# Optimization experiments

Measured on AMD Instinct MI355X. Metric: run time of the kernel, lower is better.

The kernel has to match this reference:

```python
import jax, jax.numpy as jnp
import numpy as np

B, S, H = 2, 2048, 2048
NH, NKV, D = 32, 8, 64
N_REP = NH // NKV  # 4
THETA = 10000.0


def _rotate_half(x):
    x1, x2 = jnp.split(x, 2, axis=-1)
    return jnp.concatenate([-x2, x1], axis=-1)


def _apply_rope(q, k, position_ids):
    # q: [B,NH,S,D], k: [B,NKV,S,D], position_ids: [B,S]
    inv_freq = 1.0 / (THETA ** (jnp.arange(0, D, 2, dtype=jnp.float32) / D))  # [D/2]
    ang = position_ids[:, None, :, None].astype(jnp.float32) * inv_freq      # [B,1,S,D/2]
    cos = jnp.concatenate([jnp.cos(ang), jnp.cos(ang)], axis=-1)             # [B,1,S,D]
    sin = jnp.concatenate([jnp.sin(ang), jnp.sin(ang)], axis=-1)
    q = q * cos + _rotate_half(q) * sin
    k = k * cos + _rotate_half(k) * sin
    return q, k


def setup_inputs() -> dict:
    key = jax.random.key(0)
    k1, k2, k3, k4 = jax.random.split(key, 4)
    hidden_states = jax.random.normal(k1, (B, S, H), dtype=jnp.float32)
    position_ids = jnp.broadcast_to(jnp.arange(S, dtype=jnp.int64 if jax.config.jax_enable_x64 else jnp.int32)[None, :], (B, S))
    Wq = jax.random.normal(k2, (H, NH * D), dtype=jnp.float32) * 0.02
    Wkv = jax.random.normal(k3, (H, NKV * 2 * D), dtype=jnp.float32) * 0.02
    Wo = jax.random.normal(k4, (H, H), dtype=jnp.float32) * 0.02
    return {"hidden_states": hidden_states, "position_ids": position_ids,
            "Wq": Wq, "Wkv": Wkv, "Wo": Wo}


def reference(hidden_states, position_ids, Wq, Wkv, Wo):
    b, s, _ = hidden_states.shape
    # fused QKV projections (Linear, no bias)
    q = (hidden_states @ Wq).reshape(b, s, NH, D).transpose(0, 2, 1, 3)      # [B,NH,S,D]
    kv = (hidden_states @ Wkv).reshape(b, s, NKV, 2, D)
    k = kv[:, :, :, 0, :].transpose(0, 2, 1, 3)                              # [B,NKV,S,D]
    v = kv[:, :, :, 1, :].transpose(0, 2, 1, 3)                              # [B,NKV,S,D]
    # rotary embedding
    q, k = _apply_rope(q, k, position_ids)
    # GQA: repeat_interleave K/V heads
    k = jnp.repeat(k, N_REP, axis=1)                                         # [B,NH,S,D]
    v = jnp.repeat(v, N_REP, axis=1)
    # causal SDPA (eval mode: dropout_p = 0)
    scale = 1.0 / np.sqrt(D)
    scores = jnp.einsum('bhqd,bhkd->bhqk', q, k) * scale                     # [B,NH,S,S]
    causal = jnp.tril(jnp.ones((s, s), dtype=bool))
    scores = jnp.where(causal[None, None], scores, jnp.finfo(scores.dtype).min)
    probs = jax.nn.softmax(scores, axis=-1)
    ctx = jnp.einsum('bhqk,bhkd->bhqd', probs, v)                            # [B,NH,S,D]
    ctx = ctx.transpose(0, 2, 1, 3).reshape(b, s, H)
    return ctx @ Wo
```

## Files before the change

kernel.cpp:

```cpp
#include <hip/hip_runtime.h>

typedef __bf16 bf16_t;
typedef __bf16 bf16x8 __attribute__((ext_vector_type(8)));
typedef __bf16 bf16x4 __attribute__((ext_vector_type(4)));
typedef float f32x4 __attribute__((ext_vector_type(4)));

#define DEV static __device__ __forceinline__

DEV void gload16(const void* g, void* lds) {
  __builtin_amdgcn_global_load_lds((__attribute__((address_space(1))) void*)g,
                                   (__attribute__((address_space(3))) void*)lds, 16, 0, 0);
}

DEV f32x4 mfma16(bf16x8 a, bf16x8 b, f32x4 c) {
  return __builtin_amdgcn_mfma_f32_16x16x32_bf16(a, b, c, 0, 0, 0);
}

__global__ __launch_bounds__(256) void k_cvt_bf16(const float* __restrict__ in,
                                                  bf16_t* __restrict__ out, int n) {
  int i = (blockIdx.x * 256 + threadIdx.x) * 4;
  if (i + 3 < n) {
    float4 v = *(const float4*)(in + i);
    bf16x4 o;
    o[0] = (bf16_t)v.x; o[1] = (bf16_t)v.y; o[2] = (bf16_t)v.z; o[3] = (bf16_t)v.w;
    *(bf16x4*)(out + i) = o;
  }
}

__global__ __launch_bounds__(256) void k_transpose(const float* __restrict__ in,
                                                   bf16_t* __restrict__ out, int R, int C) {
  __shared__ float tile[32][33];
  const int tx = threadIdx.x & 31, ty = threadIdx.x >> 5;
  const int rb = blockIdx.y * 32, cb = blockIdx.x * 32;
#pragma unroll
  for (int i = 0; i < 32; i += 8)
    tile[ty + i][tx] = in[(size_t)(rb + ty + i) * C + (cb + tx)];
  __syncthreads();
#pragma unroll
  for (int i = 0; i < 32; i += 8)
    out[(size_t)(cb + ty + i) * R + (rb + tx)] = (bf16_t)tile[tx][ty + i];
}

__global__ __launch_bounds__(256) void k_rope_table(const int* __restrict__ pos_ids,
                                                    float2* __restrict__ tbl) {
  const int token = blockIdx.x * 8 + (threadIdx.x >> 5);
  const int d2 = threadIdx.x & 31;
  const float p = (float)pos_ids[token];
  const float freq = exp2f(-(float)d2 / 32.0f * log2f(10000.0f));
  const float a = p * freq;
  tbl[token * 32 + d2] = make_float2(cosf(a), sinf(a));
}

#define STAGE_A(bi, st, h)                                                      \
  do {                                                                          \
    const bf16_t* _s = gA + (size_t)(brow + (h) * 128 + r0) * gK + (st) * 64 + l0 * 8; \
    gload16(_s, &As[bi][((h) * 1024 + tid) * 8]);                               \
    gload16(_s + (size_t)64 * gK, &As[bi][((h) * 1024 + 512 + tid) * 8]);       \
  } while (0)

#define STAGE_B(bi, st, h)                                                      \
  do {                                                                          \
    const bf16_t* _s = gB + (size_t)(bcol + (h) * 128 + r0) * gK + (st) * 64 + l0 * 8; \
    gload16(_s, &Bs[bi][((h) * 1024 + tid) * 8]);                               \
    gload16(_s + (size_t)64 * gK, &Bs[bi][((h) * 1024 + 512 + tid) * 8]);       \
  } while (0)

#define LOADA(bi, mh)                                                           \
  _Pragma("unroll")                                                             \
  for (int mq = 0; mq < 4; ++mq) {                                              \
    const int R = wm * 128 + (mh) * 64 + mq * 16 + c15;                         \
    af[mq][0] = *(const bf16x8*)(&As[bi][(R * 8 + (g ^ (R & 7))) * 8]);         \
    af[mq][1] = *(const bf16x8*)(&As[bi][(R * 8 + ((4 + g) ^ (R & 7))) * 8]);   \
  }

#define LOADB(bi, nh)                                                           \
  _Pragma("unroll")                                                             \
  for (int nq = 0; nq < 2; ++nq) {                                              \
    const int R = wn * 64 + ((nh) * 2 + nq) * 16 + c15;                         \
    bfr[nq][0] = *(const bf16x8*)(&Bs[bi][(R * 8 + (g ^ (R & 7))) * 8]);        \
    bfr[nq][1] = *(const bf16x8*)(&Bs[bi][(R * 8 + ((4 + g) ^ (R & 7))) * 8]);  \
  }

#define MFMAQ(mh, nh)                                                           \
  _Pragma("unroll")                                                             \
  for (int nq = 0; nq < 2; ++nq)                                                \
    _Pragma("unroll")                                                           \
    for (int mq = 0; mq < 4; ++mq)                                              \
      acc[(mh) * 4 + mq][(nh) * 2 + nq] =                                       \
          mfma16(af[mq][1], bfr[nq][1],                                         \
                 mfma16(af[mq][0], bfr[nq][0], acc[(mh) * 4 + mq][(nh) * 2 + nq]));

#define PH_MID()                                            \
  __builtin_amdgcn_s_barrier();                             \
  asm volatile("s_waitcnt lgkmcnt(0)" ::: "memory");        \
  __builtin_amdgcn_sched_barrier(0);                        \
  __builtin_amdgcn_s_setprio(1)

#define PH_END()                                            \
  __builtin_amdgcn_s_setprio(0);                            \
  __builtin_amdgcn_s_barrier()

template <int MODE>
__global__ __launch_bounds__(512, 2) void k_gemm256(
    const bf16_t* __restrict__ gA, const bf16_t* __restrict__ gB,
    int gK, int NBX,
    float* __restrict__ C, int ldc,
    const float2* __restrict__ tbl,
    bf16_t* __restrict__ Qp, bf16_t* __restrict__ Kp, bf16_t* __restrict__ Vt) {
  __shared__ __align__(16) bf16_t As[2][256 * 64];
  __shared__ __align__(16) bf16_t Bs[2][256 * 64];
  const int tid = threadIdx.x;
  const int lane = tid & 63, w = tid >> 6;
  const int c15 = lane & 15, g = lane >> 4;
  const int wm = w >> 2, wn = w & 3;

  const int cpx = (int)gridDim.x >> 3;
  const int u = ((int)blockIdx.x & 7) * cpx + ((int)blockIdx.x >> 3);
  const int bx = u % NBX, by = u / NBX;
  const int brow = by * 256, bcol = bx * 256;

  const int r0 = tid >> 3, p0 = tid & 7;
  const int l0 = p0 ^ (r0 & 7);

  const f32x4 fzero = {0.f, 0.f, 0.f, 0.f};
  f32x4 acc[8][4];
#pragma unroll
  for (int m = 0; m < 8; ++m)
#pragma unroll
    for (int n = 0; n < 4; ++n) acc[m][n] = fzero;

  const int NT = gK >> 6;

  STAGE_A(0, 0, 0); STAGE_A(0, 0, 1); STAGE_B(0, 0, 0); STAGE_B(0, 0, 1);
  STAGE_A(1, 1, 0);
  asm volatile("s_waitcnt vmcnt(2)" ::: "memory");
  __builtin_amdgcn_s_barrier();

  for (int t = 0; t < NT; ++t) {
    const int bi = t & 1, oi = bi ^ 1;
    const int st1 = (t + 1 < NT) ? t + 1 : NT - 1;
    const int st2 = (t + 2 < NT) ? t + 2 : NT - 1;
    bf16x8 af[4][2], bfr[2][2];

    LOADA(bi, 0);
    LOADB(bi, 0);
    STAGE_A(oi, st1, 1);
    STAGE_B(oi, st1, 0);
    PH_MID();
    MFMAQ(0, 0);
    PH_END();

    LOADB(bi, 1);
    STAGE_B(oi, st1, 1);
    PH_MID();
    MFMAQ(0, 1);
    PH_END();

    LOADA(bi, 1);
    LOADB(bi, 0);
    PH_MID();
    MFMAQ(1, 0);
    PH_END();

    LOADB(bi, 1);
    STAGE_A(bi, st2, 0);
    asm volatile("s_waitcnt vmcnt(2)" ::: "memory");
    PH_MID();
    MFMAQ(1, 1);
    PH_END();
  }

  if constexpr (MODE == 0) {
#pragma unroll
    for (int m = 0; m < 8; ++m)
#pragma unroll
      for (int n = 0; n < 4; ++n)
#pragma unroll
        for (int r = 0; r < 4; ++r) {
          const int row = brow + wm * 128 + m * 16 + g * 4 + r;
          const int col = bcol + wn * 64 + n * 16 + c15;
          C[(size_t)row * ldc + col] = acc[m][n][r];
        }
  } else {
    const int seg = bcol + wn * 64;
    const int wrow = brow + wm * 128;
    const float QSCALE = 0.125f * 1.44269504088896340736f;
    if (seg < 2048) {
      const int hq = seg >> 6;
#pragma unroll
      for (int m = 0; m < 8; ++m)
#pragma unroll
        for (int r = 0; r < 4; ++r) {
          const int row = wrow + m * 16 + g * 4 + r;
          const int bb = row >> 11, s = row & 2047;
          const float2 cs0 = tbl[row * 32 + c15];
          const float2 cs1 = tbl[row * 32 + 16 + c15];
          bf16_t* dst = Qp + (((size_t)bb * 32 + hq) * 2048 + s) * 64;
          dst[c15]      = (bf16_t)((acc[m][0][r] * cs0.x - acc[m][2][r] * cs0.y) * QSCALE);
          dst[32 + c15] = (bf16_t)((acc[m][2][r] * cs0.x + acc[m][0][r] * cs0.y) * QSCALE);
          dst[16 + c15] = (bf16_t)((acc[m][1][r] * cs1.x - acc[m][3][r] * cs1.y) * QSCALE);
          dst[48 + c15] = (bf16_t)((acc[m][3][r] * cs1.x + acc[m][1][r] * cs1.y) * QSCALE);
        }
    } else {
      const int cc = seg - 2048;
      const int kvh = cc >> 7;
      if (((cc >> 6) & 1) == 0) {
#pragma unroll
        for (int m = 0; m < 8; ++m)
#pragma unroll
          for (int r = 0; r < 4; ++r) {
            const int row = wrow + m * 16 + g * 4 + r;
            const int bb = row >> 11, s = row & 2047;
            const float2 cs0 = tbl[row * 32 + c15];
            const float2 cs1 = tbl[row * 32 + 16 + c15];
            bf16_t* dst = Kp + (((size_t)bb * 8 + kvh) * 2048 + s) * 64;
            dst[c15]      = (bf16_t)(acc[m][0][r] * cs0.x - acc[m][2][r] * cs0.y);
            dst[32 + c15] = (bf16_t)(acc[m][2][r] * cs0.x + acc[m][0][r] * cs0.y);
            dst[16 + c15] = (bf16_t)(acc[m][1][r] * cs1.x - acc[m][3][r] * cs1.y);
            dst[48 + c15] = (bf16_t)(acc[m][3][r] * cs1.x + acc[m][1][r] * cs1.y);
          }
      } else {
#pragma unroll
        for (int m = 0; m < 8; ++m) {
          const int row0 = wrow + m * 16 + g * 4;
          const int bb = row0 >> 11, s0 = row0 & 2047;
#pragma unroll
          for (int n = 0; n < 4; ++n) {
            bf16x4 o;
#pragma unroll
            for (int r = 0; r < 4; ++r) o[r] = (bf16_t)acc[m][n][r];
            const int d = n * 16 + c15;
            *(bf16x4*)(Vt + ((size_t)(bb * 8 + kvh) * 64 + d) * 2048 + s0) = o;
          }
        }
      }
    }
  }
}

__global__ __launch_bounds__(256, 3) void k_attn(const bf16_t* __restrict__ Qp,
                                                 const bf16_t* __restrict__ Kp,
                                                 const bf16_t* __restrict__ Vt,
                                                 bf16_t* __restrict__ ctx) {
  const int wgid = blockIdx.x;
  const int gidx = wgid & 15;
  const int j    = wgid >> 4;
  const int b = gidx >> 3, kvh = gidx & 7;
  const int qs = 63 - j;
  const int tid = threadIdx.x, lane = tid & 63, w = tid >> 6;
  const int h = kvh * 4 + w;
  const int c15 = lane & 15, g = lane >> 4;

  __shared__ __align__(16) bf16_t Ks[2][64 * 64];
  __shared__ __align__(16) bf16_t Vs[2][64 * 64];
  __shared__ __align__(16) bf16_t Pw[4][32 * 64];
  bf16_t* pw = &Pw[w][0];

  const int q0 = qs * 32;

  bf16x8 aq[2][2];
#pragma unroll
  for (int m = 0; m < 2; ++m) {
    const bf16_t* Qrow = Qp + (((size_t)b * 32 + h) * 2048 + q0 + m * 16 + c15) * 64;
    aq[m][0] = *(const bf16x8*)(Qrow + g * 8);
    aq[m][1] = *(const bf16x8*)(Qrow + 32 + g * 8);
  }
  asm volatile("s_waitcnt vmcnt(0)" ::: "memory");

  const bf16_t* Kb = Kp + ((size_t)b * 8 + kvh) * (size_t)(2048 * 64);
  const bf16_t* Vb = Vt + ((size_t)b * 8 + kvh) * (size_t)(64 * 2048);

  const int c0 = tid,      r0 = c0 >> 3, l0 = (c0 & 7) ^ (r0 & 7);
  const int c1 = tid + 256, r1 = c1 >> 3, l1 = (c1 & 7) ^ (r1 & 7);
  const int dst0 = (w * 64) * 8, dst1 = (w * 64 + 256) * 8;

  const f32x4 fzero = {0.f, 0.f, 0.f, 0.f};
  f32x4 acc[2][4];
  f32x4 lsum[2];
#pragma unroll
  for (int m = 0; m < 2; ++m) {
    lsum[m] = fzero;
#pragma unroll
    for (int n = 0; n < 4; ++n) acc[m][n] = fzero;
  }
  bf16x8 bones;
#pragma unroll
  for (int j2 = 0; j2 < 8; ++j2) bones[j2] = (bf16_t)1.0f;

  const int ntw = qs / 2 + 1;

  gload16(Kb + (size_t)r0 * 64 + l0 * 8, &Ks[0][dst0]);
  gload16(Kb + (size_t)r1 * 64 + l1 * 8, &Ks[0][dst1]);
  gload16(Vb + (size_t)r0 * 2048 + l0 * 8, &Vs[0][dst0]);
  gload16(Vb + (size_t)r1 * 2048 + l1 * 8, &Vs[0][dst1]);

  for (int t = 0; t < ntw; ++t) {
    const int kvbase = t * 64;
    const int tnb = (t + 1 < ntw ? t + 1 : t) * 64;
    const int nb = (t + 1) & 1, cb = t & 1;

    gload16(Kb + (size_t)(tnb + r0) * 64 + l0 * 8, &Ks[nb][dst0]);
    gload16(Kb + (size_t)(tnb + r1) * 64 + l1 * 8, &Ks[nb][dst1]);
    gload16(Vb + (size_t)r0 * 2048 + tnb + l0 * 8, &Vs[nb][dst0]);
    gload16(Vb + (size_t)r1 * 2048 + tnb + l1 * 8, &Vs[nb][dst1]);
    asm volatile("s_waitcnt vmcnt(4)" ::: "memory");
    __builtin_amdgcn_s_barrier();

    const bf16_t* Kc = &Ks[cb][0];
    f32x4 sv[2][4];
    __builtin_amdgcn_s_setprio(1);
#pragma unroll
    for (int n = 0; n < 4; ++n) {
      const int row = n * 16 + c15;
      const bf16x8 bk0 = *(const bf16x8*)(Kc + row * 64 + ((g ^ (row & 7)) << 3));
      const bf16x8 bk1 = *(const bf16x8*)(Kc + row * 64 + (((4 + g) ^ (row & 7)) << 3));
      sv[0][n] = mfma16(aq[0][1], bk1, mfma16(aq[0][0], bk0, fzero));
      sv[1][n] = mfma16(aq[1][1], bk1, mfma16(aq[1][0], bk0, fzero));
    }
    __builtin_amdgcn_s_setprio(0);

    if (kvbase + 63 > q0) {
#pragma unroll
      for (int n = 0; n < 4; ++n)
#pragma unroll
        for (int r = 0; r < 4; ++r) {
          const int col = kvbase + n * 16 + c15;
          if (col > q0 + g * 4 + r)      sv[0][n][r] = -1e30f;
          if (col > q0 + 16 + g * 4 + r) sv[1][n][r] = -1e30f;
        }
    }
#pragma unroll
    for (int n = 0; n < 4; ++n)
#pragma unroll
      for (int r = 0; r < 4; ++r) {
        const int col = n * 16 + c15;
        const int rp0 = g * 4 + r, rp1 = 16 + g * 4 + r;
        pw[rp0 * 64 + ((((col >> 3) ^ (rp0 & 7)) << 3) | (col & 7))] = (bf16_t)exp2f(sv[0][n][r]);
        pw[rp1 * 64 + ((((col >> 3) ^ (rp1 & 7)) << 3) | (col & 7))] = (bf16_t)exp2f(sv[1][n][r]);
      }
    asm volatile("s_waitcnt lgkmcnt(0)" ::: "memory");
    __builtin_amdgcn_sched_barrier(0);

    bf16x8 ap[2][2];
#pragma unroll
    for (int m = 0; m < 2; ++m) {
      const int q = m * 16 + c15;
      ap[m][0] = *(const bf16x8*)(pw + q * 64 + ((g ^ (q & 7)) << 3));
      ap[m][1] = *(const bf16x8*)(pw + q * 64 + (((4 + g) ^ (q & 7)) << 3));
    }
    const bf16_t* Vc = &Vs[cb][0];
    __builtin_amdgcn_s_setprio(1);
#pragma unroll
    for (int m = 0; m < 2; ++m)
      lsum[m] = mfma16(ap[m][1], bones, mfma16(ap[m][0], bones, lsum[m]));
#pragma unroll
    for (int n = 0; n < 4; ++n) {
      const int row = n * 16 + c15;
      const bf16x8 bv0 = *(const bf16x8*)(Vc + row * 64 + ((g ^ (row & 7)) << 3));
      const bf16x8 bv1 = *(const bf16x8*)(Vc + row * 64 + (((4 + g) ^ (row & 7)) << 3));
#pragma unroll
      for (int m = 0; m < 2; ++m)
        acc[m][n] = mfma16(ap[m][1], bv1, mfma16(ap[m][0], bv0, acc[m][n]));
    }
    __builtin_amdgcn_s_setprio(0);
    __builtin_amdgcn_s_barrier();
  }

#pragma unroll
  for (int m = 0; m < 2; ++m) {
    float inv[4];
#pragma unroll
    for (int r = 0; r < 4; ++r) inv[r] = 1.0f / lsum[m][r];
#pragma unroll
    for (int n = 0; n < 4; ++n)
#pragma unroll
      for (int r = 0; r < 4; ++r) {
        const int rowq = q0 + m * 16 + g * 4 + r;
        const int col = h * 64 + n * 16 + c15;
        ctx[((size_t)b * 2048 + rowq) * 2048 + col] = (bf16_t)(acc[m][n][r] * inv[r]);
      }
  }
}

extern "C" void kernel_launch(void* const* d_in, const int* in_sizes, int n_in,
                              void* d_out, int out_size, void* d_ws, size_t ws_size,
                              hipStream_t stream) {
  const float* hs  = (const float*)d_in[0];
  const int*   pos = (const int*)d_in[1];
  const float* Wq  = (const float*)d_in[2];
  const float* Wkv = (const float*)d_in[3];
  const float* Wo  = (const float*)d_in[4];
  float* out = (float*)d_out;
  (void)in_sizes; (void)n_in; (void)out_size; (void)ws_size;

  char* p = (char*)d_ws;
  bf16_t* Xbf   = (bf16_t*)p; p += (size_t)4096 * 2048 * 2;
  bf16_t* Wqkvt = (bf16_t*)p; p += (size_t)3072 * 2048 * 2;
  bf16_t* Wot   = (bf16_t*)p; p += (size_t)2048 * 2048 * 2;
  float2* tbl   = (float2*)p; p += (size_t)4096 * 32 * 8;
  bf16_t* Qp    = (bf16_t*)p; p += (size_t)2 * 32 * 2048 * 64 * 2;
  bf16_t* Kp    = (bf16_t*)p; p += (size_t)2 * 8 * 2048 * 64 * 2;
  bf16_t* Vt    = (bf16_t*)p; p += (size_t)2 * 8 * 64 * 2048 * 2;
  bf16_t* ctx   = (bf16_t*)p; p += (size_t)4096 * 2048 * 2;

  k_cvt_bf16<<<8192, 256, 0, stream>>>(hs, Xbf, 4096 * 2048);
  k_transpose<<<dim3(64, 64), 256, 0, stream>>>(Wq, Wqkvt, 2048, 2048);
  k_transpose<<<dim3(32, 64), 256, 0, stream>>>(Wkv, Wqkvt + (size_t)2048 * 2048, 2048, 1024);
  k_transpose<<<dim3(64, 64), 256, 0, stream>>>(Wo, Wot, 2048, 2048);
  k_rope_table<<<512, 256, 0, stream>>>(pos, tbl);
  k_gemm256<1><<<192, 512, 0, stream>>>(Xbf, Wqkvt, 2048, 12,
                                        nullptr, 0, tbl, Qp, Kp, Vt);
  k_attn<<<1024, 256, 0, stream>>>(Qp, Kp, Vt, ctx);
  k_gemm256<0><<<128, 512, 0, stream>>>(ctx, Wot, 2048, 8,
                                        out, 2048, nullptr, nullptr, nullptr, nullptr);
}
```

Measured before the change: 214.9 us.

## Merge prep kernels into one launch and retile output GEMM to 256x128

Folds the bf16 conversion, three weight transposes and the RoPE table build into a single k_prep launch, so four kernel launches and their tail gaps disappear. The QKV GEMM becomes a specialized kernel with constant K and grid width. The output projection gets its own kernel with 256x128 tiles and 256 blocks instead of 128 blocks of 256x256, which fills more CUs on the 256-CU device. The price is a smaller B tile per block, so each block reuses loaded data less.

Result: faster. 188.8 us (-12.2%).

```diff
diff --git a/kernel.cpp b/kernel.cpp
--- a/kernel.cpp
+++ b/kernel.cpp
@@ -16,22 +16,10 @@
   return __builtin_amdgcn_mfma_f32_16x16x32_bf16(a, b, c, 0, 0, 0);
 }
 
-__global__ __launch_bounds__(256) void k_cvt_bf16(const float* __restrict__ in,
-                                                  bf16_t* __restrict__ out, int n) {
-  int i = (blockIdx.x * 256 + threadIdx.x) * 4;
-  if (i + 3 < n) {
-    float4 v = *(const float4*)(in + i);
-    bf16x4 o;
-    o[0] = (bf16_t)v.x; o[1] = (bf16_t)v.y; o[2] = (bf16_t)v.z; o[3] = (bf16_t)v.w;
-    *(bf16x4*)(out + i) = o;
-  }
-}
-
-__global__ __launch_bounds__(256) void k_transpose(const float* __restrict__ in,
-                                                   bf16_t* __restrict__ out, int R, int C) {
-  __shared__ float tile[32][33];
-  const int tx = threadIdx.x & 31, ty = threadIdx.x >> 5;
-  const int rb = blockIdx.y * 32, cb = blockIdx.x * 32;
+DEV void transpose_blk(const float* __restrict__ in, bf16_t* __restrict__ out,
+                       int R, int C, int bx, int by, int tid, float (*tile)[33]) {
+  const int tx = tid & 31, ty = tid >> 5;
+  const int rb = by * 32, cb = bx * 32;
 #pragma unroll
   for (int i = 0; i < 32; i += 8)
     tile[ty + i][tx] = in[(size_t)(rb + ty + i) * C + (cb + tx)];
@@ -41,15 +29,52 @@
     out[(size_t)(cb + ty + i) * R + (rb + tx)] = (bf16_t)tile[tx][ty + i];
 }
 
-__global__ __launch_bounds__(256) void k_rope_table(const int* __restrict__ pos_ids,
-                                                    float2* __restrict__ tbl) {
-  const int token = blockIdx.x * 8 + (threadIdx.x >> 5);
-  const int d2 = threadIdx.x & 31;
-  const float p = (float)pos_ids[token];
-  const float freq = exp2f(-(float)d2 / 32.0f * log2f(10000.0f));
-  const float a = p * freq;
-  tbl[token * 32 + d2] = make_float2(cosf(a), sinf(a));
-}
+__global__ __launch_bounds__(256) void k_prep(const float* __restrict__ hs,
+                                              bf16_t* __restrict__ Xbf,
+                                              const float* __restrict__ Wq,
+                                              const float* __restrict__ Wkv,
+                                              const float* __restrict__ Wo,
+                                              bf16_t* __restrict__ Wqkvt,
+                                              bf16_t* __restrict__ Wot,
+                                              const int* __restrict__ pos_ids,
+                                              float2* __restrict__ tbl) {
+  __shared__ float tile[32][33];
+  const int bid = blockIdx.x, tid = threadIdx.x;
+  if (bid < 8192) {
+    const int i = (bid * 256 + tid) * 4;
+    float4 v = *(const float4*)(hs + i);
+    bf16x4 o;
+    o[0] = (bf16_t)v.x; o[1] = (bf16_t)v.y; o[2] = (bf16_t)v.z; o[3] = (bf16_t)v.w;
+    *(bf16x4*)(Xbf + i) = o;
+  } else if (bid < 8192 + 512) {
+    const int token = (bid - 8192) * 8 + (tid >> 5);
+    const int d2 = tid & 31;
+    const float p = (float)pos_ids[token];
+    const float freq = exp2f(-(float)d2 / 32.0f * log2f(10000.0f));
+    const float a = p * freq;
+    tbl[token * 32 + d2] = make_float2(cosf(a), sinf(a));
+  } else if (bid < 8192 + 512 + 4096) {
+    const int local = bid - (8192 + 512);
+    transpose_blk(Wq, Wqkvt, 2048, 2048, local & 63, local >> 6, tid, tile);
+  } else if (bid < 8192 + 512 + 4096 + 2048) {
+    const int local = bid - (8192 + 512 + 4096);
+    transpose_blk(Wkv, Wqkvt + (size_t)2048 * 2048, 2048, 1024,
+                  local & 31, local >> 5, tid, tile);
+  } else {
+    const int local = bid - (8192 + 512 + 4096 + 2048);
+    transpose_blk(Wo, Wot, 2048, 2048, local & 63, local >> 6, tid, tile);
+  }
+}
+
+#define PH_MID()                                            \
+  __builtin_amdgcn_s_barrier();                             \
+  asm volatile("s_waitcnt lgkmcnt(0)" ::: "memory");        \
+  __builtin_amdgcn_sched_barrier(0);                        \
+  __builtin_amdgcn_s_setprio(1)
+
+#define PH_END()                                            \
+  __builtin_amdgcn_s_setprio(0);                            \
+  __builtin_amdgcn_s_barrier()
 
 #define STAGE_A(bi, st, h)                                                      \
   do {                                                                          \
@@ -90,25 +115,13 @@
           mfma16(af[mq][1], bfr[nq][1],                                         \
                  mfma16(af[mq][0], bfr[nq][0], acc[(mh) * 4 + mq][(nh) * 2 + nq]));
 
-#define PH_MID()                                            \
-  __builtin_amdgcn_s_barrier();                             \
-  asm volatile("s_waitcnt lgkmcnt(0)" ::: "memory");        \
-  __builtin_amdgcn_sched_barrier(0);                        \
-  __builtin_amdgcn_s_setprio(1)
-
-#define PH_END()                                            \
-  __builtin_amdgcn_s_setprio(0);                            \
-  __builtin_amdgcn_s_barrier()
-
-template <int MODE>
-__global__ __launch_bounds__(512, 2) void k_gemm256(
+__global__ __launch_bounds__(512, 2) void k_gemm_qkv(
     const bf16_t* __restrict__ gA, const bf16_t* __restrict__ gB,
-    int gK, int NBX,
-    float* __restrict__ C, int ldc,
     const float2* __restrict__ tbl,
     bf16_t* __restrict__ Qp, bf16_t* __restrict__ Kp, bf16_t* __restrict__ Vt) {
   __shared__ __align__(16) bf16_t As[2][256 * 64];
   __shared__ __align__(16) bf16_t Bs[2][256 * 64];
+  const int gK = 2048, NBX = 12;
   const int tid = threadIdx.x;
   const int lane = tid & 63, w = tid >> 6;
   const int c15 = lane & 15, g = lane >> 4;
@@ -170,23 +183,29 @@
     PH_END();
   }
 
-  if constexpr (MODE == 0) {
+  const int seg = bcol + wn * 64;
+  const int wrow = brow + wm * 128;
+  const float QSCALE = 0.125f * 1.44269504088896340736f;
+  if (seg < 2048) {
+    const int hq = seg >> 6;
 #pragma unroll
     for (int m = 0; m < 8; ++m)
 #pragma unroll
-      for (int n = 0; n < 4; ++n)
-#pragma unroll
-        for (int r = 0; r < 4; ++r) {
-          const int row = brow + wm * 128 + m * 16 + g * 4 + r;
-          const int col = bcol + wn * 64 + n * 16 + c15;
-          C[(size_t)row * ldc + col] = acc[m][n][r];
-        }
+      for (int r = 0; r < 4; ++r) {
+        const int row = wrow + m * 16 + g * 4 + r;
+        const int bb = row >> 11, s = row & 2047;
+        const float2 cs0 = tbl[row * 32 + c15];
+        const float2 cs1 = tbl[row * 32 + 16 + c15];
+        bf16_t* dst = Qp + (((size_t)bb * 32 + hq) * 2048 + s) * 64;
+        dst[c15]      = (bf16_t)((acc[m][0][r] * cs0.x - acc[m][2][r] * cs0.y) * QSCALE);
+        dst[32 + c15] = (bf16_t)((acc[m][2][r] * cs0.x + acc[m][0][r] * cs0.y) * QSCALE);
+        dst[16 + c15] = (bf16_t)((acc[m][1][r] * cs1.x - acc[m][3][r] * cs1.y) * QSCALE);
+        dst[48 + c15] = (bf16_t)((acc[m][3][r] * cs1.x + acc[m][1][r] * cs1.y) * QSCALE);
+      }
   } else {
-    const int seg = bcol + wn * 64;
-    const int wrow = brow + wm * 128;
-    const float QSCALE = 0.125f * 1.44269504088896340736f;
-    if (seg < 2048) {
-      const int hq = seg >> 6;
+    const int cc = seg - 2048;
+    const int kvh = cc >> 7;
+    if (((cc >> 6) & 1) == 0) {
 #pragma unroll
       for (int m = 0; m < 8; ++m)
 #pragma unroll
@@ -195,47 +214,126 @@
           const int bb = row >> 11, s = row & 2047;
           const float2 cs0 = tbl[row * 32 + c15];
           const float2 cs1 = tbl[row * 32 + 16 + c15];
-          bf16_t* dst = Qp + (((size_t)bb * 32 + hq) * 2048 + s) * 64;
-          dst[c15]      = (bf16_t)((acc[m][0][r] * cs0.x - acc[m][2][r] * cs0.y) * QSCALE);
-          dst[32 + c15] = (bf16_t)((acc[m][2][r] * cs0.x + acc[m][0][r] * cs0.y) * QSCALE);
-          dst[16 + c15] = (bf16_t)((acc[m][1][r] * cs1.x - acc[m][3][r] * cs1.y) * QSCALE);
-          dst[48 + c15] = (bf16_t)((acc[m][3][r] * cs1.x + acc[m][1][r] * cs1.y) * QSCALE);
+          bf16_t* dst = Kp + (((size_t)bb * 8 + kvh) * 2048 + s) * 64;
+          dst[c15]      = (bf16_t)(acc[m][0][r] * cs0.x - acc[m][2][r] * cs0.y);
+          dst[32 + c15] = (bf16_t)(acc[m][2][r] * cs0.x + acc[m][0][r] * cs0.y);
+          dst[16 + c15] = (bf16_t)(acc[m][1][r] * cs1.x - acc[m][3][r] * cs1.y);
+          dst[48 + c15] = (bf16_t)(acc[m][3][r] * cs1.x + acc[m][1][r] * cs1.y);
         }
     } else {
-      const int cc = seg - 2048;
-      const int kvh = cc >> 7;
-      if (((cc >> 6) & 1) == 0) {
-#pragma unroll
-        for (int m = 0; m < 8; ++m)
-#pragma unroll
-          for (int r = 0; r < 4; ++r) {
-            const int row = wrow + m * 16 + g * 4 + r;
-            const int bb = row >> 11, s = row & 2047;
-            const float2 cs0 = tbl[row * 32 + c15];
-            const float2 cs1 = tbl[row * 32 + 16 + c15];
-            bf16_t* dst = Kp + (((size_t)bb * 8 + kvh) * 2048 + s) * 64;
-            dst[c15]      = (bf16_t)(acc[m][0][r] * cs0.x - acc[m][2][r] * cs0.y);
-            dst[32 + c15] = (bf16_t)(acc[m][2][r] * cs0.x + acc[m][0][r] * cs0.y);
-            dst[16 + c15] = (bf16_t)(acc[m][1][r] * cs1.x - acc[m][3][r] * cs1.y);
-            dst[48 + c15] = (bf16_t)(acc[m][3][r] * cs1.x + acc[m][1][r] * cs1.y);
-          }
-      } else {
-#pragma unroll
-        for (int m = 0; m < 8; ++m) {
-          const int row0 = wrow + m * 16 + g * 4;
-          const int bb = row0 >> 11, s0 = row0 & 2047;
-#pragma unroll
-          for (int n = 0; n < 4; ++n) {
-            bf16x4 o;
-#pragma unroll
-            for (int r = 0; r < 4; ++r) o[r] = (bf16_t)acc[m][n][r];
-            const int d = n * 16 + c15;
-            *(bf16x4*)(Vt + ((size_t)(bb * 8 + kvh) * 64 + d) * 2048 + s0) = o;
-          }
+#pragma unroll
+      for (int m = 0; m < 8; ++m) {
+        const int row0 = wrow + m * 16 + g * 4;
+        const int bb = row0 >> 11, s0 = row0 & 2047;
+#pragma unroll
+        for (int n = 0; n < 4; ++n) {
+          bf16x4 o;
+#pragma unroll
+          for (int r = 0; r < 4; ++r) o[r] = (bf16_t)acc[m][n][r];
+          const int d = n * 16 + c15;
+          *(bf16x4*)(Vt + ((size_t)(bb * 8 + kvh) * 64 + d) * 2048 + s0) = o;
         }
       }
     }
   }
+}
+
+#define OSTAGE_A(bi, st, h)                                                     \
+  do {                                                                          \
+    const bf16_t* _s = gA + (size_t)(brow + (h) * 128 + r0) * gK + (st) * 64 + l0 * 8; \
+    gload16(_s, &As[bi][((h) * 1024 + tid) * 8]);                               \
+    gload16(_s + (size_t)64 * gK, &As[bi][((h) * 1024 + 512 + tid) * 8]);       \
+  } while (0)
+
+#define OSTAGE_B(bi, st)                                                        \
+  do {                                                                          \
+    const bf16_t* _s = gB + (size_t)(bcol + r0) * gK + (st) * 64 + l0 * 8;      \
+    gload16(_s, &Bs[bi][tid * 8]);                                              \
+    gload16(_s + (size_t)64 * gK, &Bs[bi][(512 + tid) * 8]);                    \
+  } while (0)
+
+#define OLOADB(bi)                                                              \
+  _Pragma("unroll")                                                             \
+  for (int nq = 0; nq < 2; ++nq) {                                              \
+    const int R = wn * 32 + nq * 16 + c15;                                      \
+    bfr[nq][0] = *(const bf16x8*)(&Bs[bi][(R * 8 + (g ^ (R & 7))) * 8]);        \
+    bfr[nq][1] = *(const bf16x8*)(&Bs[bi][(R * 8 + ((4 + g) ^ (R & 7))) * 8]);  \
+  }
+
+#define OMFMAQ(mh)                                                              \
+  _Pragma("unroll")                                                             \
+  for (int nq = 0; nq < 2; ++nq)                                                \
+    _Pragma("unroll")                                                           \
+    for (int mq = 0; mq < 4; ++mq)                                              \
+      acc[(mh) * 4 + mq][nq] =                                                  \
+          mfma16(af[mq][1], bfr[nq][1],                                         \
+                 mfma16(af[mq][0], bfr[nq][0], acc[(mh) * 4 + mq][nq]));
+
+__global__ __launch_bounds__(512, 2) void k_gemm_out(
+    const bf16_t* __restrict__ gA, const bf16_t* __restrict__ gB,
+    float* __restrict__ C) {
+  __shared__ __align__(16) bf16_t As[2][256 * 64];
+  __shared__ __align__(16) bf16_t Bs[2][128 * 64];
+  const int gK = 2048, NBX = 16, ldc = 2048;
+  const int tid = threadIdx.x;
+  const int lane = tid & 63, w = tid >> 6;
+  const int c15 = lane & 15, g = lane >> 4;
+  const int wm = w >> 2, wn = w & 3;
+
+  const int cpx = (int)gridDim.x >> 3;
+  const int u = ((int)blockIdx.x & 7) * cpx + ((int)blockIdx.x >> 3);
+  const int bx = u % NBX, by = u / NBX;
+  const int brow = by * 256, bcol = bx * 128;
+
+  const int r0 = tid >> 3, p0 = tid & 7;
+  const int l0 = p0 ^ (r0 & 7);
+
+  const f32x4 fzero = {0.f, 0.f, 0.f, 0.f};
+  f32x4 acc[8][2];
+#pragma unroll
+  for (int m = 0; m < 8; ++m)
+#pragma unroll
+    for (int n = 0; n < 2; ++n) acc[m][n] = fzero;
+
+  const int NT = gK >> 6;
+
+  OSTAGE_A(0, 0, 0); OSTAGE_A(0, 0, 1); OSTAGE_B(0, 0);
+  OSTAGE_A(1, 1, 0); OSTAGE_B(1, 1);
+  asm volatile("s_waitcnt vmcnt(4)" ::: "memory");
+  __builtin_amdgcn_s_barrier();
+
+  for (int t = 0; t < NT; ++t) {
+    const int bi = t & 1, oi = bi ^ 1;
+    const int st1 = (t + 1 < NT) ? t + 1 : NT - 1;
+    const int st2 = (t + 2 < NT) ? t + 2 : NT - 1;
+    bf16x8 af[4][2], bfr[2][2];
+
+    LOADA(bi, 0);
+    OLOADB(bi);
+    OSTAGE_A(oi, st1, 1);
+    PH_MID();
+    OMFMAQ(0);
+    PH_END();
+
+    LOADA(bi, 1);
+    OSTAGE_A(bi, st2, 0);
+    OSTAGE_B(bi, st2);
+    asm volatile("s_waitcnt vmcnt(4)" ::: "memory");
+    PH_MID();
+    OMFMAQ(1);
+    PH_END();
+  }
+
+#pragma unroll
+  for (int m = 0; m < 8; ++m)
+#pragma unroll
+    for (int n = 0; n < 2; ++n)
+#pragma unroll
+      for (int r = 0; r < 4; ++r) {
+        const int row = brow + wm * 128 + m * 16 + g * 4 + r;
+        const int col = bcol + wn * 32 + n * 16 + c15;
+        C[(size_t)row * ldc + col] = acc[m][n][r];
+      }
 }
 
 __global__ __launch_bounds__(256, 3) void k_attn(const bf16_t* __restrict__ Qp,
@@ -403,14 +501,8 @@
   bf16_t* Vt    = (bf16_t*)p; p += (size_t)2 * 8 * 64 * 2048 * 2;
   bf16_t* ctx   = (bf16_t*)p; p += (size_t)4096 * 2048 * 2;
 
-  k_cvt_bf16<<<8192, 256, 0, stream>>>(hs, Xbf, 4096 * 2048);
-  k_transpose<<<dim3(64, 64), 256, 0, stream>>>(Wq, Wqkvt, 2048, 2048);
-  k_transpose<<<dim3(32, 64), 256, 0, stream>>>(Wkv, Wqkvt + (size_t)2048 * 2048, 2048, 1024);
-  k_transpose<<<dim3(64, 64), 256, 0, stream>>>(Wo, Wot, 2048, 2048);
-  k_rope_table<<<512, 256, 0, stream>>>(pos, tbl);
-  k_gemm256<1><<<192, 512, 0, stream>>>(Xbf, Wqkvt, 2048, 12,
-                                        nullptr, 0, tbl, Qp, Kp, Vt);
+  k_prep<<<18944, 256, 0, stream>>>(hs, Xbf, Wq, Wkv, Wo, Wqkvt, Wot, pos, tbl);
+  k_gemm_qkv<<<192, 512, 0, stream>>>(Xbf, Wqkvt, tbl, Qp, Kp, Vt);
   k_attn<<<1024, 256, 0, stream>>>(Qp, Kp, Vt, ctx);
-  k_gemm256<0><<<128, 512, 0, stream>>>(ctx, Wot, 2048, 8,
-                                        out, 2048, nullptr, nullptr, nullptr, nullptr);
-}
+  k_gemm_out<<<256, 512, 0, stream>>>(ctx, Wot, out);
+}
```
